# Performance work log

Measured on AMD Instinct MI355X. Metric: run time of the kernel, lower is better.

Reference implementation:

```python
import jax, jax.numpy as jnp
import numpy as np

# pywt db4 analysis filters (dec_lo, dec_hi), length 8
DEC_LO = np.array([-0.010597401784997278, 0.032883011666982945, 0.030841381835986965,
                   -0.18703481171888114, -0.02798376941698385, 0.6308807679295904,
                   0.7148465705525415, 0.23037781330885523], dtype=np.float32)
DEC_HI = np.array([-0.23037781330885523, 0.7148465705525415, -0.6308807679295904,
                   -0.02798376941698385, 0.18703481171888114, 0.030841381835986965,
                   -0.032883011666982945, -0.010597401784997278], dtype=np.float32)


def setup_inputs() -> dict:
    key = jax.random.key(0)
    x = jax.random.normal(key, (32, 3, 512, 512), dtype=jnp.float32)
    dec = jnp.stack([jnp.asarray(DEC_LO), jnp.asarray(DEC_HI)])  # (2, 8)
    return {"x": x, "dec": dec}


def _afb1d_last(x, dec):
    """Analysis filter bank along last axis: circular pad (end), stride-2
    cross-correlation with lo/hi filters. x: (..., L) -> (lo, hi) each (..., L//2)."""
    L = x.shape[-1]
    taps = dec.shape[-1]
    pad = taps - 1
    xp = jnp.concatenate([x, x[..., :pad]], axis=-1)          # circular pad at end
    flat = xp.reshape(-1, 1, xp.shape[-1])                    # (N, 1, L+pad)
    out = jax.lax.conv_general_dilated(
        flat, dec[:, None, :], window_strides=(2,), padding='VALID',
        dimension_numbers=('NCH', 'OIH', 'NCH'))              # (N, 2, L//2)
    out = out.reshape(*x.shape[:-1], 2, L // 2)
    return out[..., 0, :], out[..., 1, :]


def reference(x, dec):
    B, C, H, W = x.shape
    xr = x.reshape(B * C, H, W)
    # row pass (along W)
    lo_w, hi_w = _afb1d_last(xr, dec)                         # (BC, H, W//2)
    # column pass (along H): move H to last axis
    lo_t = jnp.swapaxes(lo_w, -2, -1)                         # (BC, W//2, H)
    hi_t = jnp.swapaxes(hi_w, -2, -1)
    ll, lh = _afb1d_last(lo_t, dec)                           # (BC, W//2, H//2)
    hl, hh = _afb1d_last(hi_t, dec)
    coeffs = jnp.stack([ll, lh, hl, hh], axis=1)              # (BC, 4, W//2, H//2)
    coeffs = jnp.swapaxes(coeffs, -2, -1)                     # (BC, 4, H//2, W//2)
    return coeffs.reshape(B, C * 4, H // 2, W // 2)
```

## Files before the change

### kernel.cpp

```cpp
#include <hip/hip_runtime.h>


#define TI 16
#define TJ 64
#define PR (2*TI + 6)
#define PC 136
#define HH 512
#define WW 512

typedef float v4f __attribute__((ext_vector_type(4)));

__global__ __launch_bounds__(256)
void dwt2d_db4_kernel(const float* __restrict__ x,
                      const float* __restrict__ dec,
                      float* __restrict__ out) {
    __shared__ __align__(16) float sm_x[PR][PC];
    __shared__ __align__(16) float sm_lo[PR][TJ];
    __shared__ __align__(16) float sm_hi[PR][TJ];

    const int tid = threadIdx.x;
    const int jt  = blockIdx.x;
    const int it  = blockIdx.y;
    const int bc  = blockIdx.z;

    const int rowBase = it * (2 * TI);
    const int colBase = jt * (2 * TJ);

    float flo[8], fhi[8];
#pragma unroll
    for (int k = 0; k < 8; ++k) { flo[k] = dec[k]; fhi[k] = dec[8 + k]; }

    const float* xb = x + (size_t)bc * HH * WW;

    {
        const int C4 = PC / 4;
        for (int idx = tid; idx < PR * C4; idx += 256) {
            int r  = idx / C4;
            int c4 = idx - r * C4;
            int gr = rowBase + r; if (gr >= HH) gr -= HH;
            int gc = colBase + 4 * c4;
            const float* src = xb + gr * WW;
            float4 v;
            if (gc + 3 < WW) {
                v = *(const float4*)(src + gc);
            } else {
                v = make_float4(src[gc & (WW-1)], src[(gc+1) & (WW-1)],
                                src[(gc+2) & (WW-1)], src[(gc+3) & (WW-1)]);
            }
            *(float4*)&sm_x[r][4 * c4] = v;
        }
    }
    __syncthreads();

    for (int task = tid; task < PR * (TJ / 2); task += 256) {
        int r = task >> 5;
        int t = task & 31;
        const float* xr = &sm_x[r][4 * t];
        float4 v0 = *(const float4*)(xr);
        float4 v1 = *(const float4*)(xr + 4);
        float4 v2 = *(const float4*)(xr + 8);
        float w[12] = { v0.x, v0.y, v0.z, v0.w,
                        v1.x, v1.y, v1.z, v1.w,
                        v2.x, v2.y, v2.z, v2.w };
        float lo0 = 0.f, hi0 = 0.f, lo1 = 0.f, hi1 = 0.f;
#pragma unroll
        for (int q = 0; q < 8; ++q) {
            lo0 += w[q]     * flo[q];
            hi0 += w[q]     * fhi[q];
            lo1 += w[q + 2] * flo[q];
            hi1 += w[q + 2] * fhi[q];
        }
        *(float2*)&sm_lo[r][2 * t] = make_float2(lo0, lo1);
        *(float2*)&sm_hi[r][2 * t] = make_float2(hi0, hi1);
    }
    __syncthreads();

    {
        int i  = tid >> 4;
        int jb = tid & 15;
        int j0 = 4 * jb;
        float llx=0.f, lly=0.f, llz=0.f, llw=0.f;
        float lhx=0.f, lhy=0.f, lhz=0.f, lhw=0.f;
        float hlx=0.f, hly=0.f, hlz=0.f, hlw=0.f;
        float hhx=0.f, hhy=0.f, hhz=0.f, hhw=0.f;
#pragma unroll
        for (int p = 0; p < 8; ++p) {
            float4 a = *(const float4*)&sm_lo[2 * i + p][j0];
            float4 b = *(const float4*)&sm_hi[2 * i + p][j0];
            float cl = flo[p], ch = fhi[p];
            llx += a.x * cl; lly += a.y * cl; llz += a.z * cl; llw += a.w * cl;
            lhx += a.x * ch; lhy += a.y * ch; lhz += a.z * ch; lhw += a.w * ch;
            hlx += b.x * cl; hly += b.y * cl; hlz += b.z * cl; hlw += b.w * cl;
            hhx += b.x * ch; hhy += b.y * ch; hhz += b.z * ch; hhw += b.w * ch;
        }
        int oi = it * TI + i;
        int oj = jt * TJ + j0;
        size_t base = ((size_t)(bc * 4) * 256 + oi) * 256 + oj;
        v4f ll = { llx, lly, llz, llw };
        v4f lh = { lhx, lhy, lhz, lhw };
        v4f hl = { hlx, hly, hlz, hlw };
        v4f hh = { hhx, hhy, hhz, hhw };
        __builtin_nontemporal_store(ll, (v4f*)&out[base]);
        __builtin_nontemporal_store(lh, (v4f*)&out[base + 1 * 65536]);
        __builtin_nontemporal_store(hl, (v4f*)&out[base + 2 * 65536]);
        __builtin_nontemporal_store(hh, (v4f*)&out[base + 3 * 65536]);
    }
}

extern "C" void kernel_launch(void* const* d_in, const int* in_sizes, int n_in,
                              void* d_out, int out_size, void* d_ws, size_t ws_size,
                              hipStream_t stream) {
    const float* x   = (const float*)d_in[0];
    const float* dec = (const float*)d_in[1];
    float* out = (float*)d_out;

    dim3 grid(256 / TJ, 256 / TI, 96);
    dim3 block(256);
    dwt2d_db4_kernel<<<grid, block, 0, stream>>>(x, dec, out);
}
```

Baseline: 180.3 us.

## Load input rows directly from global memory, dropping shared staging tile

The row-pass threads now read their 12-element windows straight from global memory with float4 loads, so the shared-memory input tile, its fill loop and one barrier are gone. Launch bounds also request 8 blocks per multiprocessor, helped by the smaller shared footprint. The cost is overlapping global reads, since each 8-element halo is fetched by neighbouring threads, which must be absorbed by the cache. There is also added register pressure from the occupancy hint.

```diff
diff --git a/kernel.cpp b/kernel.cpp
--- a/kernel.cpp
+++ b/kernel.cpp
@@ -4,17 +4,15 @@
 #define TI 16
 #define TJ 64
 #define PR (2*TI + 6)
-#define PC 136
 #define HH 512
 #define WW 512
 
 typedef float v4f __attribute__((ext_vector_type(4)));
 
-__global__ __launch_bounds__(256)
+__global__ __launch_bounds__(256, 8)
 void dwt2d_db4_kernel(const float* __restrict__ x,
                       const float* __restrict__ dec,
                       float* __restrict__ out) {
-    __shared__ __align__(16) float sm_x[PR][PC];
     __shared__ __align__(16) float sm_lo[PR][TJ];
     __shared__ __align__(16) float sm_hi[PR][TJ];
 
@@ -32,36 +30,26 @@
 
     const float* xb = x + (size_t)bc * HH * WW;
 
-    {
-        const int C4 = PC / 4;
-        for (int idx = tid; idx < PR * C4; idx += 256) {
-            int r  = idx / C4;
-            int c4 = idx - r * C4;
-            int gr = rowBase + r; if (gr >= HH) gr -= HH;
-            int gc = colBase + 4 * c4;
-            const float* src = xb + gr * WW;
-            float4 v;
-            if (gc + 3 < WW) {
-                v = *(const float4*)(src + gc);
-            } else {
-                v = make_float4(src[gc & (WW-1)], src[(gc+1) & (WW-1)],
-                                src[(gc+2) & (WW-1)], src[(gc+3) & (WW-1)]);
-            }
-            *(float4*)&sm_x[r][4 * c4] = v;
-        }
-    }
-    __syncthreads();
-
     for (int task = tid; task < PR * (TJ / 2); task += 256) {
         int r = task >> 5;
         int t = task & 31;
-        const float* xr = &sm_x[r][4 * t];
-        float4 v0 = *(const float4*)(xr);
-        float4 v1 = *(const float4*)(xr + 4);
-        float4 v2 = *(const float4*)(xr + 8);
-        float w[12] = { v0.x, v0.y, v0.z, v0.w,
-                        v1.x, v1.y, v1.z, v1.w,
-                        v2.x, v2.y, v2.z, v2.w };
+        int gr = rowBase + r; if (gr >= HH) gr -= HH;
+        const float* src = xb + gr * WW;
+        int gc = colBase + 4 * t;
+
+        float w[12];
+        if (gc + 11 < WW) {
+            float4 v0 = *(const float4*)(src + gc);
+            float4 v1 = *(const float4*)(src + gc + 4);
+            float4 v2 = *(const float4*)(src + gc + 8);
+            w[0]=v0.x; w[1]=v0.y; w[2]=v0.z;  w[3]=v0.w;
+            w[4]=v1.x; w[5]=v1.y; w[6]=v1.z;  w[7]=v1.w;
+            w[8]=v2.x; w[9]=v2.y; w[10]=v2.z; w[11]=v2.w;
+        } else {
+#pragma unroll
+            for (int k = 0; k < 12; ++k) w[k] = src[(gc + k) & (WW - 1)];
+        }
+
         float lo0 = 0.f, hi0 = 0.f, lo1 = 0.f, hi1 = 0.f;
 #pragma unroll
         for (int q = 0; q < 8; ++q) {
```

Result: slower. 195.5 us (+8.4%).

## Load input tile directly into LDS and halve row tile height

Applied to the files above, without the earlier changes.

The input halo tile is now staged with `__builtin_amdgcn_global_load_lds`, which writes 16-byte chunks straight into a flat shared array. This replaces the float4 register round-trip and the branchy wrap handling; column wraparound becomes a simple subtraction. The output rows per block drop from 16 to 8, which halves LDS use and doubles the block count, and the column-pass stores shrink from float4 to float2. The aim is to cut load latency and raise occupancy, at the cost of more redundant halo rows read per output and narrower stores.

```diff
diff --git a/kernel.cpp b/kernel.cpp
--- a/kernel.cpp
+++ b/kernel.cpp
@@ -1,27 +1,31 @@
 #include <hip/hip_runtime.h>
 
 
-#define TI 16
+#define TI 8
 #define TJ 64
 #define PR (2*TI + 6)
 #define PC 136
+#define NG ((PR * PC) / 4)
 #define HH 512
 #define WW 512
 
-typedef float v4f __attribute__((ext_vector_type(4)));
+typedef float v2f __attribute__((ext_vector_type(2)));
+typedef const __attribute__((address_space(1))) void gas_t;
+typedef __attribute__((address_space(3))) void las_t;
 
 __global__ __launch_bounds__(256)
 void dwt2d_db4_kernel(const float* __restrict__ x,
                       const float* __restrict__ dec,
                       float* __restrict__ out) {
-    __shared__ __align__(16) float sm_x[PR][PC];
+    __shared__ __align__(16) float sm_x[PR * PC];
     __shared__ __align__(16) float sm_lo[PR][TJ];
     __shared__ __align__(16) float sm_hi[PR][TJ];
 
-    const int tid = threadIdx.x;
-    const int jt  = blockIdx.x;
-    const int it  = blockIdx.y;
-    const int bc  = blockIdx.z;
+    const int tid  = threadIdx.x;
+    const int wid  = tid >> 6;
+    const int jt   = blockIdx.x;
+    const int it   = blockIdx.y;
+    const int bc   = blockIdx.z;
 
     const int rowBase = it * (2 * TI);
     const int colBase = jt * (2 * TJ);
@@ -32,22 +36,17 @@
 
     const float* xb = x + (size_t)bc * HH * WW;
 
-    {
-        const int C4 = PC / 4;
-        for (int idx = tid; idx < PR * C4; idx += 256) {
-            int r  = idx / C4;
-            int c4 = idx - r * C4;
-            int gr = rowBase + r; if (gr >= HH) gr -= HH;
-            int gc = colBase + 4 * c4;
-            const float* src = xb + gr * WW;
-            float4 v;
-            if (gc + 3 < WW) {
-                v = *(const float4*)(src + gc);
-            } else {
-                v = make_float4(src[gc & (WW-1)], src[(gc+1) & (WW-1)],
-                                src[(gc+2) & (WW-1)], src[(gc+3) & (WW-1)]);
-            }
-            *(float4*)&sm_x[r][4 * c4] = v;
+#pragma unroll
+    for (int k = 0; k < 3; ++k) {
+        int g = k * 256 + tid;
+        las_t* lp = (las_t*)((char*)sm_x + k * 4096 + wid * 1024);
+        if (g < NG) {
+            int r  = g / 34;
+            int c4 = g - r * 34;
+            int gr = rowBase + r;  if (gr >= HH) gr -= HH;
+            int gc = colBase + 4 * c4; if (gc >= WW) gc -= WW;
+            const float* gp = xb + gr * WW + gc;
+            __builtin_amdgcn_global_load_lds((gas_t*)gp, lp, 16, 0, 0);
         }
     }
     __syncthreads();
@@ -55,7 +54,7 @@
     for (int task = tid; task < PR * (TJ / 2); task += 256) {
         int r = task >> 5;
         int t = task & 31;
-        const float* xr = &sm_x[r][4 * t];
+        const float* xr = &sm_x[r * PC + 4 * t];
         float4 v0 = *(const float4*)(xr);
         float4 v1 = *(const float4*)(xr + 4);
         float4 v2 = *(const float4*)(xr + 8);
@@ -76,34 +75,29 @@
     __syncthreads();
 
     {
-        int i  = tid >> 4;
-        int jb = tid & 15;
-        int j0 = 4 * jb;
-        float llx=0.f, lly=0.f, llz=0.f, llw=0.f;
-        float lhx=0.f, lhy=0.f, lhz=0.f, lhw=0.f;
-        float hlx=0.f, hly=0.f, hlz=0.f, hlw=0.f;
-        float hhx=0.f, hhy=0.f, hhz=0.f, hhw=0.f;
+        int i  = tid >> 5;
+        int j0 = (tid & 31) * 2;
+        float ll0=0.f, ll1=0.f, lh0=0.f, lh1=0.f;
+        float hl0=0.f, hl1=0.f, hh0=0.f, hh1=0.f;
 #pragma unroll
         for (int p = 0; p < 8; ++p) {
-            float4 a = *(const float4*)&sm_lo[2 * i + p][j0];
-            float4 b = *(const float4*)&sm_hi[2 * i + p][j0];
+            float2 a = *(const float2*)&sm_lo[2 * i + p][j0];
+            float2 b = *(const float2*)&sm_hi[2 * i + p][j0];
             float cl = flo[p], ch = fhi[p];
-            llx += a.x * cl; lly += a.y * cl; llz += a.z * cl; llw += a.w * cl;
-            lhx += a.x * ch; lhy += a.y * ch; lhz += a.z * ch; lhw += a.w * ch;
-            hlx += b.x * cl; hly += b.y * cl; hlz += b.z * cl; hlw += b.w * cl;
-            hhx += b.x * ch; hhy += b.y * ch; hhz += b.z * ch; hhw += b.w * ch;
+            ll0 += a.x * cl; ll1 += a.y * cl;
+            lh0 += a.x * ch; lh1 += a.y * ch;
+            hl0 += b.x * cl; hl1 += b.y * cl;
+            hh0 += b.x * ch; hh1 += b.y * ch;
         }
         int oi = it * TI + i;
         int oj = jt * TJ + j0;
         size_t base = ((size_t)(bc * 4) * 256 + oi) * 256 + oj;
-        v4f ll = { llx, lly, llz, llw };
-        v4f lh = { lhx, lhy, lhz, lhw };
-        v4f hl = { hlx, hly, hlz, hlw };
-        v4f hh = { hhx, hhy, hhz, hhw };
-        __builtin_nontemporal_store(ll, (v4f*)&out[base]);
-        __builtin_nontemporal_store(lh, (v4f*)&out[base + 1 * 65536]);
-        __builtin_nontemporal_store(hl, (v4f*)&out[base + 2 * 65536]);
-        __builtin_nontemporal_store(hh, (v4f*)&out[base + 3 * 65536]);
+        v2f ll = { ll0, ll1 }, lh = { lh0, lh1 };
+        v2f hl = { hl0, hl1 }, hh = { hh0, hh1 };
+        __builtin_nontemporal_store(ll, (v2f*)&out[base]);
+        __builtin_nontemporal_store(lh, (v2f*)&out[base + 1 * 65536]);
+        __builtin_nontemporal_store(hl, (v2f*)&out[base + 2 * 65536]);
+        __builtin_nontemporal_store(hh, (v2f*)&out[base + 3 * 65536]);
     }
 }
 
```

New measurement: 173.0 us. 1.04x faster.
